# Kernel optimization log

Measured on AMD Instinct MI355X. Metric: run time of the kernel, lower is better.

The kernel has to match this reference:

```python
import jax, jax.numpy as jnp
import numpy as np

NUM_Q_HEADS = 32
NUM_KV_HEADS = 8
HEAD_DIM = 128
HIDDEN = 4096
EPS = 1e-6
ROPE_THETA = 1e6


def _rmsnorm(t, w):
    # per-head RMSNorm over last dim (head_dim), as in skip_rmsnorm with residual=None
    var = jnp.mean(t * t, axis=-1, keepdims=True)
    return t * jax.lax.rsqrt(var + EPS) * w


def _rotate_half(t):
    h = t.shape[-1] // 2
    return jnp.concatenate([-t[..., h:], t[..., :h]], axis=-1)


def setup_inputs() -> dict:
    key = jax.random.key(0)
    ks = jax.random.split(key, 4)
    B, S = 2, 1024
    x = jax.random.normal(ks[0], (B, S, HIDDEN), jnp.float32)
    q_proj_w = jax.random.normal(ks[1], (HIDDEN, NUM_Q_HEADS * HEAD_DIM), jnp.float32) * 0.02
    kv_proj_w = jax.random.normal(ks[2], (HIDDEN, 2 * NUM_KV_HEADS * HEAD_DIM), jnp.float32) * 0.02
    o_proj_w = jax.random.normal(ks[3], (NUM_Q_HEADS * HEAD_DIM, HIDDEN), jnp.float32) * 0.02
    q_norm_w = jnp.ones((HEAD_DIM,), jnp.float32)
    k_norm_w = jnp.ones((HEAD_DIM,), jnp.float32)
    # real rotate-half RoPE tables, shape [S, head_dim]
    inv_freq = 1.0 / (ROPE_THETA ** (jnp.arange(0, HEAD_DIM, 2, dtype=jnp.float32) / HEAD_DIM))
    freqs = jnp.arange(S, dtype=jnp.float32)[:, None] * inv_freq[None, :]  # [S, hd/2]
    emb = jnp.concatenate([freqs, freqs], axis=-1)  # [S, hd]
    cos, sin = jnp.cos(emb), jnp.sin(emb)
    kv_buffer = jnp.zeros((16384, 2 * NUM_KV_HEADS, HEAD_DIM), jnp.float32)
    cur_select_index = jnp.arange(B * S, dtype=jnp.int32)
    return {"x": x, "q_proj_w": q_proj_w, "kv_proj_w": kv_proj_w, "o_proj_w": o_proj_w,
            "q_norm_w": q_norm_w, "k_norm_w": k_norm_w, "cos": cos, "sin": sin,
            "kv_buffer": kv_buffer, "cur_select_index": cur_select_index}


def reference(x, q_proj_w, kv_proj_w, o_proj_w, q_norm_w, k_norm_w, cos, sin, kv_buffer, cur_select_index):
    B, S, _ = x.shape
    T = B * S
    xf = x.reshape(T, HIDDEN)
    # projections (weights stored as [in, out])
    xq = (xf @ q_proj_w).reshape(T, NUM_Q_HEADS, HEAD_DIM)
    xkv = xf @ kv_proj_w
    xk = xkv[:, : NUM_KV_HEADS * HEAD_DIM].reshape(T, NUM_KV_HEADS, HEAD_DIM)
    xv = xkv[:, NUM_KV_HEADS * HEAD_DIM:].reshape(T, NUM_KV_HEADS, HEAD_DIM)
    # per-head RMSNorm (Qwen3 q/k norm)
    xq = _rmsnorm(xq, q_norm_w)
    xk = _rmsnorm(xk, k_norm_w)
    # RoPE (cos/sin are [S, hd], tiled over batch, broadcast over heads)
    cos_t = jnp.tile(cos, (B, 1))[:, None, :]  # [T,1,hd]
    sin_t = jnp.tile(sin, (B, 1))[:, None, :]
    xq = xq * cos_t + _rotate_half(xq) * sin_t
    xk = xk * cos_t + _rotate_half(xk) * sin_t
    # paged KV-cache scatter update (update_kv_buffer)
    combined_kv = jnp.concatenate([xk, xv], axis=1)  # [T, 2*Hk, hd]
    buf = kv_buffer.at[cur_select_index].set(combined_kv)
    # ragged causal flash attention (equal per-request lengths here), GQA expand
    rep = NUM_Q_HEADS // NUM_KV_HEADS
    q = xq.reshape(B, S, NUM_Q_HEADS, HEAD_DIM)
    k = jnp.repeat(xk.reshape(B, S, NUM_KV_HEADS, HEAD_DIM), rep, axis=2)
    v = jnp.repeat(xv.reshape(B, S, NUM_KV_HEADS, HEAD_DIM), rep, axis=2)
    scale = HEAD_DIM ** -0.5
    scores = jnp.einsum('bqhd,bkhd->bhqk', q, k) * scale  # [B,H,S,S]
    causal = jnp.tril(jnp.ones((S, S), bool))
    scores = jnp.where(causal[None, None], scores, jnp.float32(-1e30))
    p = jax.nn.softmax(scores, axis=-1)
    attn = jnp.einsum('bhqk,bkhd->bqhd', p, v).reshape(B, S, NUM_Q_HEADS * HEAD_DIM)
    out = attn @ o_proj_w  # [B,S,hidden]
    return out, buf
```

## Files before the change

kernel.cpp:

```cpp
#include <hip/hip_runtime.h>

typedef float fx4 __attribute__((ext_vector_type(4)));
typedef short s16x4 __attribute__((ext_vector_type(4)));
typedef short s16x8 __attribute__((ext_vector_type(8)));
typedef __bf16 bf16x8 __attribute__((ext_vector_type(8)));

__device__ __forceinline__ short f2bf(float f) {
  unsigned u = __builtin_bit_cast(unsigned, f);
  u += 0x7fffu + ((u >> 16) & 1u);
  return (short)(u >> 16);
}

__device__ __forceinline__ bf16x8 ld8(const short* p) {
  s16x8 v = *(const s16x8*)p;
  return __builtin_bit_cast(bf16x8, v);
}

__device__ __forceinline__ void gld16(const void* g, void* l) {
  __builtin_amdgcn_global_load_lds(
      (const __attribute__((address_space(1))) unsigned*)g,
      (__attribute__((address_space(3))) unsigned*)l, 16, 0, 0);
}

template<int N> __device__ __forceinline__ void wait_vmcnt() {
  if constexpr (N == 0)      asm volatile("s_waitcnt vmcnt(0)" ::: "memory");
  else if constexpr (N == 4) asm volatile("s_waitcnt vmcnt(4)" ::: "memory");
  __builtin_amdgcn_sched_barrier(0);
}

__device__ __forceinline__ void barrier_pin() {
  __builtin_amdgcn_s_barrier();
  __builtin_amdgcn_sched_barrier(0);
}

__global__ __launch_bounds__(256) void cvt_k(const float* __restrict__ in,
                                             short* __restrict__ out) {
  int i = (blockIdx.x * 256 + threadIdx.x) * 8;
  fx4 a = *(const fx4*)(in + i);
  fx4 b = *(const fx4*)(in + i + 4);
  s16x8 w;
  w[0] = f2bf(a[0]); w[1] = f2bf(a[1]); w[2] = f2bf(a[2]); w[3] = f2bf(a[3]);
  w[4] = f2bf(b[0]); w[5] = f2bf(b[1]); w[6] = f2bf(b[2]); w[7] = f2bf(b[3]);
  *(s16x8*)(out + i) = w;
}

__global__ __launch_bounds__(256) void tr_k(const float* __restrict__ in,
    short* __restrict__ out, int K, int N) {
  __shared__ short T[64][72];
  const int ktiles = K >> 6;
  const int tk0 = (blockIdx.x % ktiles) << 6;
  const int tn0 = (blockIdx.x / ktiles) << 6;
  const int tid = threadIdx.x;
  #pragma unroll
  for (int i = 0; i < 4; ++i) {
    int idx = i * 256 + tid;
    int k = idx >> 4, n4 = (idx & 15) << 2;
    fx4 v = *(const fx4*)(in + (size_t)(tk0 + k) * N + tn0 + n4);
    #pragma unroll
    for (int j = 0; j < 4; ++j) T[n4 + j][k] = f2bf(v[j]);
  }
  __syncthreads();
  #pragma unroll
  for (int i = 0; i < 2; ++i) {
    int idx = i * 256 + tid;
    int n = idx >> 3, k8 = (idx & 7) << 3;
    *(s16x8*)(out + (size_t)(tn0 + n) * K + tk0 + k8) = *(const s16x8*)&T[n][k8];
  }
}

__global__ __launch_bounds__(256) void vtr_k(const short* __restrict__ vbp,
                                             short* __restrict__ vbt) {
  __shared__ short T[64][72];
  const int tile = blockIdx.x & 31;
  const int tt = tile & 15, dt = tile >> 4;
  const int bk = blockIdx.x >> 5;
  const int b = bk >> 3, kvh = bk & 7;
  const int t0 = tt << 6, d0 = dt << 6;
  const int tid = threadIdx.x;
  #pragma unroll
  for (int i = 0; i < 2; ++i) {
    int idx = i * 256 + tid;
    int r = idx >> 3, c8 = (idx & 7) << 3;
    s16x8 v = *(const s16x8*)(vbp + (size_t)(b * 1024 + t0 + r) * 1024 + kvh * 128 + d0 + c8);
    #pragma unroll
    for (int j = 0; j < 8; ++j) T[c8 + j][r] = v[j];
  }
  __syncthreads();
  #pragma unroll
  for (int i = 0; i < 2; ++i) {
    int idx = i * 256 + tid;
    int r = idx >> 3, c8 = (idx & 7) << 3;
    *(s16x8*)(vbt + ((size_t)(b * 8 + kvh) * 128 + d0 + r) * 1024 + t0 + c8) =
        *(const s16x8*)&T[r][c8];
  }
}

__global__ __launch_bounds__(512) void gemm8(const short* __restrict__ A,
    const short* __restrict__ Bt, float* __restrict__ Cp, int N, int K) {
  __shared__ short As[2][2][128 * 64];
  __shared__ short Bs[2][2][128 * 64];
  const int tiles_n = N >> 8;
  const int tm = blockIdx.x / tiles_n, tn = blockIdx.x % tiles_n;
  const int tid = threadIdx.x;
  const int lane = tid & 63, wv = tid >> 6;
  const int wm = (wv >> 2) << 6;
  const int wn = (wv & 3) << 5;
  const int r0 = tm << 8, c0 = tn << 8;
  const int lrow = lane & 15, lg = lane >> 4;

  auto stageA = [&](int t, int hh) {
    int k0 = t << 6, s = t & 1;
    #pragma unroll
    for (int i = 0; i < 2; ++i) {
      int c = i * 512 + tid;
      int row = c >> 3, ch = c & 7;
      gld16(A + (size_t)(r0 + hh * 128 + row) * K + k0 + ((ch ^ (row & 7)) << 3),
            &As[s][hh][(i * 512 + wv * 64) * 8]);
    }
  };
  auto stageB = [&](int t, int hh) {
    int k0 = t << 6, s = t & 1;
    #pragma unroll
    for (int i = 0; i < 2; ++i) {
      int c = i * 512 + tid;
      int row = c >> 3, ch = c & 7;
      gld16(Bt + (size_t)(c0 + hh * 128 + row) * K + k0 + ((ch ^ (row & 7)) << 3),
            &Bs[s][hh][(i * 512 + wv * 64) * 8]);
    }
  };

  fx4 acc[2][2][4][2] = {};
  bf16x8 a[4][2], b[2][2];

  auto ldA = [&](int s, int hh) {
    #pragma unroll
    for (int mf = 0; mf < 4; ++mf) {
      int lr = wm + mf * 16 + lrow;
      #pragma unroll
      for (int ks = 0; ks < 2; ++ks)
        a[mf][ks] = ld8(&As[s][hh][lr * 64 + ((((ks << 2) + lg) ^ (lr & 7)) << 3)]);
    }
  };
  auto ldB = [&](int s, int hh) {
    #pragma unroll
    for (int nf = 0; nf < 2; ++nf) {
      int lr = wn + nf * 16 + lrow;
      #pragma unroll
      for (int ks = 0; ks < 2; ++ks)
        b[nf][ks] = ld8(&Bs[s][hh][lr * 64 + ((((ks << 2) + lg) ^ (lr & 7)) << 3)]);
    }
  };

  const int nt = K >> 6;
  stageA(0, 0); stageA(0, 1); stageB(0, 0); stageB(0, 1);
  stageA(1, 0); stageB(1, 1);

  for (int t = 0; t < nt; ++t) {
    const int s = t & 1;
    if (t + 1 < nt) wait_vmcnt<4>(); else wait_vmcnt<0>();
    barrier_pin();
    ldA(s, 0); ldB(s, 0);
    if (t + 1 < nt) stageA(t + 1, 1);
    __builtin_amdgcn_s_setprio(1);
    #pragma unroll
    for (int ks = 0; ks < 2; ++ks)
      #pragma unroll
      for (int mf = 0; mf < 4; ++mf)
        #pragma unroll
        for (int nf = 0; nf < 2; ++nf)
          acc[0][0][mf][nf] = __builtin_amdgcn_mfma_f32_16x16x32_bf16(
              a[mf][ks], b[nf][ks], acc[0][0][mf][nf], 0, 0, 0);
    __builtin_amdgcn_s_setprio(0);
    barrier_pin();
    ldB(s, 1);
    if (t + 1 < nt) stageB(t + 1, 0);
    __builtin_amdgcn_s_setprio(1);
    #pragma unroll
    for (int ks = 0; ks < 2; ++ks)
      #pragma unroll
      for (int mf = 0; mf < 4; ++mf)
        #pragma unroll
        for (int nf = 0; nf < 2; ++nf)
          acc[0][1][mf][nf] = __builtin_amdgcn_mfma_f32_16x16x32_bf16(
              a[mf][ks], b[nf][ks], acc[0][1][mf][nf], 0, 0, 0);
    __builtin_amdgcn_s_setprio(0);
    barrier_pin();
    ldA(s, 1);
    if (t + 2 < nt) stageA(t + 2, 0);
    __builtin_amdgcn_s_setprio(1);
    #pragma unroll
    for (int ks = 0; ks < 2; ++ks)
      #pragma unroll
      for (int mf = 0; mf < 4; ++mf)
        #pragma unroll
        for (int nf = 0; nf < 2; ++nf)
          acc[1][1][mf][nf] = __builtin_amdgcn_mfma_f32_16x16x32_bf16(
              a[mf][ks], b[nf][ks], acc[1][1][mf][nf], 0, 0, 0);
    __builtin_amdgcn_s_setprio(0);
    barrier_pin();
    ldB(s, 0);
    if (t + 2 < nt) stageB(t + 2, 1);
    __builtin_amdgcn_s_setprio(1);
    #pragma unroll
    for (int ks = 0; ks < 2; ++ks)
      #pragma unroll
      for (int mf = 0; mf < 4; ++mf)
        #pragma unroll
        for (int nf = 0; nf < 2; ++nf)
          acc[1][0][mf][nf] = __builtin_amdgcn_mfma_f32_16x16x32_bf16(
              a[mf][ks], b[nf][ks], acc[1][0][mf][nf], 0, 0, 0);
    __builtin_amdgcn_s_setprio(0);
    barrier_pin();
  }
  const int g4 = lg << 2;
  #pragma unroll
  for (int mq = 0; mq < 2; ++mq)
    #pragma unroll
    for (int nq = 0; nq < 2; ++nq)
      #pragma unroll
      for (int mf = 0; mf < 4; ++mf)
        #pragma unroll
        for (int nf = 0; nf < 2; ++nf)
          #pragma unroll
          for (int j = 0; j < 4; ++j) {
            int row = r0 + mq * 128 + wm + mf * 16 + g4 + j;
            int col = c0 + nq * 128 + wn + nf * 16 + lrow;
            Cp[(size_t)row * N + col] = acc[mq][nq][mf][nf][j];
          }
}

__global__ __launch_bounds__(256) void gemm_k(const short* __restrict__ A,
    const short* __restrict__ Bt, float* __restrict__ Cp, int N, int K) {
  __shared__ short As[2][128 * 64];
  __shared__ short Bs[2][128 * 64];
  const int tiles_n = N >> 7;
  const int tm = blockIdx.x / tiles_n, tn = blockIdx.x % tiles_n;
  const int tid = threadIdx.x;
  const int lane = tid & 63, wv = tid >> 6;
  const int wr = (wv >> 1) << 6, wc = (wv & 1) << 6;
  const int r0 = tm << 7, c0 = tn << 7;
  const int lrow = lane & 15, lg = lane >> 4;
  fx4 acc[4][4] = {};

  auto stage = [&](int buf, int k0) {
    #pragma unroll
    for (int i = 0; i < 4; ++i) {
      int c = i * 256 + tid;
      int row = c >> 3, ch = c & 7;
      gld16(A + (size_t)(r0 + row) * K + k0 + ((ch ^ (row & 7)) << 3),
            &As[buf][(i * 256 + wv * 64) * 8]);
    }
    #pragma unroll
    for (int i = 0; i < 4; ++i) {
      int c = i * 256 + tid;
      int row = c >> 3, ch = c & 7;
      gld16(Bt + (size_t)(c0 + row) * K + k0 + ((ch ^ (row & 7)) << 3),
            &Bs[buf][(i * 256 + wv * 64) * 8]);
    }
  };

  const int nt = K >> 6;
  stage(0, 0);
  __syncthreads();
  int cur = 0;
  for (int t = 0; t < nt; ++t) {
    if (t + 1 < nt) stage(cur ^ 1, (t + 1) << 6);
    bf16x8 af[4][2], bfr[4][2];
    #pragma unroll
    for (int m = 0; m < 4; ++m) {
      int row = wr + m * 16 + lrow;
      #pragma unroll
      for (int h = 0; h < 2; ++h)
        af[m][h] = ld8(&As[cur][row * 64 + ((((h << 2) + lg) ^ (row & 7)) << 3)]);
    }
    #pragma unroll
    for (int n = 0; n < 4; ++n) {
      int row = wc + n * 16 + lrow;
      #pragma unroll
      for (int h = 0; h < 2; ++h)
        bfr[n][h] = ld8(&Bs[cur][row * 64 + ((((h << 2) + lg) ^ (row & 7)) << 3)]);
    }
    __builtin_amdgcn_s_setprio(1);
    #pragma unroll
    for (int m = 0; m < 4; ++m)
      #pragma unroll
      for (int n = 0; n < 4; ++n) {
        acc[m][n] = __builtin_amdgcn_mfma_f32_16x16x32_bf16(af[m][0], bfr[n][0], acc[m][n], 0, 0, 0);
        acc[m][n] = __builtin_amdgcn_mfma_f32_16x16x32_bf16(af[m][1], bfr[n][1], acc[m][n], 0, 0, 0);
      }
    __builtin_amdgcn_s_setprio(0);
    __syncthreads();
    cur ^= 1;
  }
  const int g4 = lg << 2;
  #pragma unroll
  for (int m = 0; m < 4; ++m)
    #pragma unroll
    for (int n = 0; n < 4; ++n)
      #pragma unroll
      for (int j = 0; j < 4; ++j) {
        int row = r0 + wr + m * 16 + g4 + j;
        int col = c0 + wc + n * 16 + lrow;
        Cp[(size_t)row * N + col] = acc[m][n][j];
      }
}

__global__ __launch_bounds__(256) void nr_k(const float* __restrict__ xqkv,
    const float* __restrict__ qnw, const float* __restrict__ knw,
    const float* __restrict__ cosb, const float* __restrict__ sinb,
    const int* __restrict__ idx,
    short* __restrict__ qb, short* __restrict__ kbp, short* __restrict__ vbp,
    float* __restrict__ bufo) {
  int rid = blockIdx.x * 4 + (threadIdx.x >> 6);
  int l = threadIdx.x & 63;
  int type, t, h;
  if (rid < 65536)      { type = 0; t = rid >> 5; h = rid & 31; }
  else if (rid < 81920) { type = 1; int r = rid - 65536; t = r >> 3; h = r & 7; }
  else                  { type = 2; int r = rid - 81920; t = r >> 3; h = r & 7; }
  int s = t & 1023;
  const float* src = xqkv + (size_t)t * 6144 +
                     ((type == 0) ? h * 128 : (type == 1) ? 4096 + h * 128
                                                          : 5120 + h * 128);
  float e0 = src[l], e1 = src[l + 64];
  float out0, out1;
  if (type < 2) {
    float ss = e0 * e0 + e1 * e1;
    #pragma unroll
    for (int off = 1; off < 64; off <<= 1) ss += __shfl_xor(ss, off);
    float r = rsqrtf(ss * (1.0f / 128.0f) + 1e-6f);
    const float* nw = (type == 0) ? qnw : knw;
    float n0 = e0 * r * nw[l], n1 = e1 * r * nw[l + 64];
    float c0 = cosb[s * 128 + l], c1 = cosb[s * 128 + 64 + l];
    float s0 = sinb[s * 128 + l], s1 = sinb[s * 128 + 64 + l];
    out0 = n0 * c0 - n1 * s0;
    out1 = n1 * c1 + n0 * s1;
  } else { out0 = e0; out1 = e1; }
  if (type == 0) {
    short* d = qb + (size_t)t * 4096 + h * 128;
    d[l] = f2bf(out0); d[l + 64] = f2bf(out1);
  } else {
    int br = idx[t];
    float* bd = bufo + (size_t)br * 2048 + (type == 1 ? 0 : 1024) + h * 128;
    bd[l] = out0; bd[l + 64] = out1;
    short* d = (type == 1) ? kbp + (size_t)t * 1024 + h * 128
                           : vbp + (size_t)t * 1024 + h * 128;
    d[l] = f2bf(out0); d[l + 64] = f2bf(out1);
  }
}

#define KLD 136
#define PLD 72

__global__ __launch_bounds__(256) void attn_k(const short* __restrict__ qb,
    const short* __restrict__ kbp, const short* __restrict__ vbt,
    short* __restrict__ ob) {
  __shared__ short Ks[64 * KLD];
  __shared__ short Vs[128 * 64];
  __shared__ short Ps[4][16 * PLD];
  const int bid = blockIdx.x;
  const int qt = 15 - (bid & 15), h = (bid >> 4) & 31, b = bid >> 9;
  const int kvh = h >> 2;
  const int tid = threadIdx.x, lane = tid & 63, w = tid >> 6;
  const int lrow = lane & 15, lg = lane >> 4, lk = lg << 3;
  const int q0 = qt << 6;
  const float SC2 = 0.088388347648318447f * 1.4426950408889634f;

  bf16x8 qf[4];
  {
    const short* qp = qb + ((size_t)(b * 1024 + q0 + w * 16 + lrow) * 32 + h) * 128 + lk;
    #pragma unroll
    for (int kb4 = 0; kb4 < 4; ++kb4) qf[kb4] = ld8(qp + kb4 * 32);
  }

  const short* vt_base = vbt + (size_t)(b * 8 + kvh) * 128 * 1024;

  const int sr = tid >> 4, sd8 = (tid & 15) << 3;
  const int vdr = tid >> 3, vch = tid & 7;
  s16x8 kreg[4], vreg[4];
  auto ldkv = [&](int kv0) {
    #pragma unroll
    for (int it = 0; it < 4; ++it) {
      int r = (it << 4) + sr;
      kreg[it] = *(const s16x8*)(kbp + ((size_t)(b * 1024 + kv0 + r) * 8 + kvh) * 128 + sd8);
      int d = (it << 5) + vdr;
      vreg[it] = *(const s16x8*)(vt_base + (size_t)d * 1024 + kv0 + (vch << 3));
    }
  };
  auto wrkv = [&]() {
    #pragma unroll
    for (int it = 0; it < 4; ++it) {
      int r = (it << 4) + sr;
      *(s16x8*)&Ks[r * KLD + sd8] = kreg[it];
      int d = (it << 5) + vdr;
      *(s16x8*)&Vs[d * 64 + ((vch ^ (d & 7)) << 3)] = vreg[it];
    }
  };

  float m[4], lsum[4];
  fx4 acc[8] = {};
  #pragma unroll
  for (int j = 0; j < 4; ++j) { m[j] = -3.0e38f; lsum[j] = 0.f; }

  ldkv(0);
  wrkv();
  __syncthreads();

  for (int kt = 0; kt <= qt; ++kt) {
    const int kv0 = kt << 6;
    if (kt < qt) ldkv((kt + 1) << 6);
    fx4 sf[4];
    #pragma unroll
    for (int nc = 0; nc < 4; ++nc) {
      fx4 z = {0.f, 0.f, 0.f, 0.f};
      sf[nc] = z;
      #pragma unroll
      for (int kb4 = 0; kb4 < 4; ++kb4) {
        bf16x8 kf = ld8(&Ks[(nc * 16 + lrow) * KLD + kb4 * 32 + lk]);
        sf[nc] = __builtin_amdgcn_mfma_f32_16x16x32_bf16(qf[kb4], kf, sf[nc], 0, 0, 0);
      }
    }
    if (kt == qt) {
      #pragma unroll
      for (int nc = 0; nc < 4; ++nc)
        #pragma unroll
        for (int j = 0; j < 4; ++j) {
          int qr = q0 + w * 16 + (lg << 2) + j;
          int kc = kv0 + nc * 16 + lrow;
          if (kc > qr) sf[nc][j] = -3.0e38f;
        }
    }
    float pm[4];
    #pragma unroll
    for (int j = 0; j < 4; ++j) pm[j] = -3.0e38f;
    #pragma unroll
    for (int nc = 0; nc < 4; ++nc)
      #pragma unroll
      for (int j = 0; j < 4; ++j) pm[j] = fmaxf(pm[j], sf[nc][j]);
    #pragma unroll
    for (int j = 0; j < 4; ++j) {
      pm[j] = fmaxf(pm[j], __shfl_xor(pm[j], 1));
      pm[j] = fmaxf(pm[j], __shfl_xor(pm[j], 2));
      pm[j] = fmaxf(pm[j], __shfl_xor(pm[j], 4));
      pm[j] = fmaxf(pm[j], __shfl_xor(pm[j], 8));
    }
    float alpha[4], rs[4];
    #pragma unroll
    for (int j = 0; j < 4; ++j) {
      float mn = fmaxf(m[j], pm[j]);
      alpha[j] = exp2f((m[j] - mn) * SC2);
      m[j] = mn;
      rs[j] = 0.f;
    }
    #pragma unroll
    for (int nc = 0; nc < 4; ++nc)
      #pragma unroll
      for (int j = 0; j < 4; ++j) {
        float p = exp2f((sf[nc][j] - m[j]) * SC2);
        rs[j] += p;
        Ps[w][((lg << 2) + j) * PLD + nc * 16 + lrow] = f2bf(p);
      }
    #pragma unroll
    for (int j = 0; j < 4; ++j) {
      rs[j] += __shfl_xor(rs[j], 1);
      rs[j] += __shfl_xor(rs[j], 2);
      rs[j] += __shfl_xor(rs[j], 4);
      rs[j] += __shfl_xor(rs[j], 8);
      lsum[j] = lsum[j] * alpha[j] + rs[j];
    }
    #pragma unroll
    for (int dg = 0; dg < 8; ++dg)
      #pragma unroll
      for (int j = 0; j < 4; ++j) acc[dg][j] *= alpha[j];
    #pragma unroll
    for (int kb2 = 0; kb2 < 2; ++kb2) {
      bf16x8 pf = ld8(&Ps[w][lrow * PLD + kb2 * 32 + lk]);
      #pragma unroll
      for (int dg = 0; dg < 8; ++dg) {
        int d = dg * 16 + lrow;
        int tch = (kb2 << 2) + lg;
        bf16x8 vf = ld8(&Vs[d * 64 + ((tch ^ (d & 7)) << 3)]);
        acc[dg] = __builtin_amdgcn_mfma_f32_16x16x32_bf16(pf, vf, acc[dg], 0, 0, 0);
      }
    }
    __syncthreads();
    if (kt < qt) {
      wrkv();
      __syncthreads();
    }
  }
  #pragma unroll
  for (int j = 0; j < 4; ++j) {
    float rl = 1.0f / lsum[j];
    int t = b * 1024 + q0 + w * 16 + (lg << 2) + j;
    short* op = ob + ((size_t)t * 32 + h) * 128;
    #pragma unroll
    for (int dg = 0; dg < 8; ++dg)
      op[dg * 16 + lrow] = f2bf(acc[dg][j] * rl);
  }
}

extern "C" void kernel_launch(void* const* d_in, const int* in_sizes, int n_in,
                              void* d_out, int out_size, void* d_ws, size_t ws_size,
                              hipStream_t stream) {
  (void)in_sizes; (void)n_in; (void)out_size; (void)ws_size;
  const float* x    = (const float*)d_in[0];
  const float* qw   = (const float*)d_in[1];
  const float* kvw  = (const float*)d_in[2];
  const float* ow   = (const float*)d_in[3];
  const float* qnw  = (const float*)d_in[4];
  const float* knw  = (const float*)d_in[5];
  const float* cosb = (const float*)d_in[6];
  const float* sinb = (const float*)d_in[7];
  const float* kvbf = (const float*)d_in[8];
  const int*   idx  = (const int*)d_in[9];

  float* outp = (float*)d_out;
  float* bufp = outp + (size_t)2048 * 4096;

  char* ws = (char*)d_ws;
  float* xqkv = (float*)ws;
  short* qb   = (short*)(ws + (size_t)2048 * 6144 * 4);
  short* kbp  = (short*)((char*)qb + (size_t)2048 * 4096 * 2);
  short* vbp  = (short*)((char*)kbp + (size_t)2048 * 1024 * 2);
  short* attnb = (short*)xqkv;
  short* owt   = (short*)((char*)xqkv + (size_t)2048 * 4096 * 2);
  short* vbt   = owt;

  short* wqkvt = (short*)bufp;
  short* xb    = (short*)((char*)bufp + (size_t)6144 * 4096 * 2);

  cvt_k<<<dim3(4096), dim3(256), 0, stream>>>(x, xb);
  tr_k<<<dim3(64 * 64), dim3(256), 0, stream>>>(qw, wqkvt, 4096, 4096);
  tr_k<<<dim3(64 * 32), dim3(256), 0, stream>>>(kvw, wqkvt + (size_t)4096 * 4096, 4096, 2048);
  gemm8<<<dim3(8 * 24), dim3(512), 0, stream>>>(xb, wqkvt, xqkv, 6144, 4096);
  hipMemcpyAsync(bufp + (size_t)2048 * 2048, kvbf + (size_t)2048 * 2048,
                 (size_t)(16384 - 2048) * 2048 * 4, hipMemcpyDeviceToDevice, stream);
  nr_k<<<dim3(98304 / 4), dim3(256), 0, stream>>>(xqkv, qnw, knw, cosb, sinb, idx,
                                                  qb, kbp, vbp, bufp);
  vtr_k<<<dim3(512), dim3(256), 0, stream>>>(vbp, vbt);
  attn_k<<<dim3(2 * 32 * 16), dim3(256), 0, stream>>>(qb, kbp, vbt, attnb);
  tr_k<<<dim3(64 * 64), dim3(256), 0, stream>>>(ow, owt, 4096, 4096);
  gemm_k<<<dim3(16 * 32), dim3(256), 0, stream>>>(attnb, owt, outp, 4096, 4096);
}
```

Baseline: 401.4 us.

## Replace output-projection GEMM with 256x128-tile, 512-thread, triple-buffered pipelined kernel

Replaces the 128x128 double-buffered o_proj GEMM with a 256x128 tile kernel using 8 waves and a three-stage LDS ring. Loads are issued two K-tiles ahead and tracked with explicit vmcnt waits, and each half of the A tile is consumed in its own phase between barriers. The aim is to hide global-load latency behind MFMA work and to reuse each B tile across more rows. In exchange it launches 256 blocks instead of 512, which may under-fill the 256 CUs, and it uses more LDS per block.

```diff
diff --git a/kernel.cpp b/kernel.cpp
--- a/kernel.cpp
+++ b/kernel.cpp
@@ -25,6 +25,7 @@
 template<int N> __device__ __forceinline__ void wait_vmcnt() {
   if constexpr (N == 0)      asm volatile("s_waitcnt vmcnt(0)" ::: "memory");
   else if constexpr (N == 4) asm volatile("s_waitcnt vmcnt(4)" ::: "memory");
+  else if constexpr (N == 6) asm volatile("s_waitcnt vmcnt(6)" ::: "memory");
   __builtin_amdgcn_sched_barrier(0);
 }
 
@@ -229,80 +230,110 @@
           }
 }
 
-__global__ __launch_bounds__(256) void gemm_k(const short* __restrict__ A,
+__global__ __launch_bounds__(512) void gemm4(const short* __restrict__ A,
     const short* __restrict__ Bt, float* __restrict__ Cp, int N, int K) {
-  __shared__ short As[2][128 * 64];
-  __shared__ short Bs[2][128 * 64];
+  __shared__ short As[3][2][128 * 64];
+  __shared__ short Bs[3][128 * 64];
   const int tiles_n = N >> 7;
   const int tm = blockIdx.x / tiles_n, tn = blockIdx.x % tiles_n;
   const int tid = threadIdx.x;
   const int lane = tid & 63, wv = tid >> 6;
-  const int wr = (wv >> 1) << 6, wc = (wv & 1) << 6;
-  const int r0 = tm << 7, c0 = tn << 7;
+  const int wm = (wv >> 2) << 6;
+  const int wn = (wv & 3) << 5;
+  const int r0 = tm << 8, c0 = tn << 7;
   const int lrow = lane & 15, lg = lane >> 4;
-  fx4 acc[4][4] = {};
-
-  auto stage = [&](int buf, int k0) {
-    #pragma unroll
-    for (int i = 0; i < 4; ++i) {
-      int c = i * 256 + tid;
+
+  auto stageA = [&](int t, int hh) {
+    int k0 = t << 6, s = t % 3;
+    #pragma unroll
+    for (int i = 0; i < 2; ++i) {
+      int c = i * 512 + tid;
       int row = c >> 3, ch = c & 7;
-      gld16(A + (size_t)(r0 + row) * K + k0 + ((ch ^ (row & 7)) << 3),
-            &As[buf][(i * 256 + wv * 64) * 8]);
-    }
-    #pragma unroll
-    for (int i = 0; i < 4; ++i) {
-      int c = i * 256 + tid;
+      gld16(A + (size_t)(r0 + hh * 128 + row) * K + k0 + ((ch ^ (row & 7)) << 3),
+            &As[s][hh][(i * 512 + wv * 64) * 8]);
+    }
+  };
+  auto stageB = [&](int t) {
+    int k0 = t << 6, s = t % 3;
+    #pragma unroll
+    for (int i = 0; i < 2; ++i) {
+      int c = i * 512 + tid;
       int row = c >> 3, ch = c & 7;
       gld16(Bt + (size_t)(c0 + row) * K + k0 + ((ch ^ (row & 7)) << 3),
-            &Bs[buf][(i * 256 + wv * 64) * 8]);
+            &Bs[s][(i * 512 + wv * 64) * 8]);
+    }
+  };
+
+  fx4 acc[2][4][2] = {};
+  bf16x8 a[4][2], b[2][2];
+
+  auto ldA = [&](int s, int hh) {
+    #pragma unroll
+    for (int mf = 0; mf < 4; ++mf) {
+      int lr = wm + mf * 16 + lrow;
+      #pragma unroll
+      for (int ks = 0; ks < 2; ++ks)
+        a[mf][ks] = ld8(&As[s][hh][lr * 64 + ((((ks << 2) + lg) ^ (lr & 7)) << 3)]);
+    }
+  };
+  auto ldB = [&](int s) {
+    #pragma unroll
+    for (int nf = 0; nf < 2; ++nf) {
+      int lr = wn + nf * 16 + lrow;
+      #pragma unroll
+      for (int ks = 0; ks < 2; ++ks)
+        b[nf][ks] = ld8(&Bs[s][lr * 64 + ((((ks << 2) + lg) ^ (lr & 7)) << 3)]);
     }
   };
 
   const int nt = K >> 6;
-  stage(0, 0);
-  __syncthreads();
-  int cur = 0;
+  stageA(0, 0); stageA(0, 1); stageB(0);
+  stageA(1, 0); stageA(1, 1); stageB(1);
+
   for (int t = 0; t < nt; ++t) {
-    if (t + 1 < nt) stage(cur ^ 1, (t + 1) << 6);
-    bf16x8 af[4][2], bfr[4][2];
-    #pragma unroll
-    for (int m = 0; m < 4; ++m) {
-      int row = wr + m * 16 + lrow;
-      #pragma unroll
-      for (int h = 0; h < 2; ++h)
-        af[m][h] = ld8(&As[cur][row * 64 + ((((h << 2) + lg) ^ (row & 7)) << 3)]);
-    }
-    #pragma unroll
-    for (int n = 0; n < 4; ++n) {
-      int row = wc + n * 16 + lrow;
-      #pragma unroll
-      for (int h = 0; h < 2; ++h)
-        bfr[n][h] = ld8(&Bs[cur][row * 64 + ((((h << 2) + lg) ^ (row & 7)) << 3)]);
-    }
+    const int s = t % 3;
+    if (t + 1 < nt) wait_vmcnt<6>(); else wait_vmcnt<0>();
+    barrier_pin();
+    ldA(s, 0); ldB(s);
+    if (t + 2 < nt) stageA(t + 2, 0);
     __builtin_amdgcn_s_setprio(1);
     #pragma unroll
-    for (int m = 0; m < 4; ++m)
-      #pragma unroll
-      for (int n = 0; n < 4; ++n) {
-        acc[m][n] = __builtin_amdgcn_mfma_f32_16x16x32_bf16(af[m][0], bfr[n][0], acc[m][n], 0, 0, 0);
-        acc[m][n] = __builtin_amdgcn_mfma_f32_16x16x32_bf16(af[m][1], bfr[n][1], acc[m][n], 0, 0, 0);
-      }
+    for (int ks = 0; ks < 2; ++ks)
+      #pragma unroll
+      for (int mf = 0; mf < 4; ++mf)
+        #pragma unroll
+        for (int nf = 0; nf < 2; ++nf)
+          acc[0][mf][nf] = __builtin_amdgcn_mfma_f32_16x16x32_bf16(
+              a[mf][ks], b[nf][ks], acc[0][mf][nf], 0, 0, 0);
     __builtin_amdgcn_s_setprio(0);
-    __syncthreads();
-    cur ^= 1;
+    barrier_pin();
+    ldA(s, 1);
+    if (t + 2 < nt) { stageA(t + 2, 1); stageB(t + 2); }
+    __builtin_amdgcn_s_setprio(1);
+    #pragma unroll
+    for (int ks = 0; ks < 2; ++ks)
+      #pragma unroll
+      for (int mf = 0; mf < 4; ++mf)
+        #pragma unroll
+        for (int nf = 0; nf < 2; ++nf)
+          acc[1][mf][nf] = __builtin_amdgcn_mfma_f32_16x16x32_bf16(
+              a[mf][ks], b[nf][ks], acc[1][mf][nf], 0, 0, 0);
+    __builtin_amdgcn_s_setprio(0);
+    barrier_pin();
   }
   const int g4 = lg << 2;
   #pragma unroll
-  for (int m = 0; m < 4; ++m)
-    #pragma unroll
-    for (int n = 0; n < 4; ++n)
-      #pragma unroll
-      for (int j = 0; j < 4; ++j) {
-        int row = r0 + wr + m * 16 + g4 + j;
-        int col = c0 + wc + n * 16 + lrow;
-        Cp[(size_t)row * N + col] = acc[m][n][j];
-      }
+  for (int mh = 0; mh < 2; ++mh)
+    #pragma unroll
+    for (int mf = 0; mf < 4; ++mf)
+      #pragma unroll
+      for (int nf = 0; nf < 2; ++nf)
+        #pragma unroll
+        for (int j = 0; j < 4; ++j) {
+          int row = r0 + mh * 128 + wm + mf * 16 + g4 + j;
+          int col = c0 + wn + nf * 16 + lrow;
+          Cp[(size_t)row * N + col] = acc[mh][mf][nf][j];
+        }
 }
 
 __global__ __launch_bounds__(256) void nr_k(const float* __restrict__ xqkv,
@@ -540,5 +571,5 @@
   vtr_k<<<dim3(512), dim3(256), 0, stream>>>(vbp, vbt);
   attn_k<<<dim3(2 * 32 * 16), dim3(256), 0, stream>>>(qb, kbp, vbt, attnb);
   tr_k<<<dim3(64 * 64), dim3(256), 0, stream>>>(ow, owt, 4096, 4096);
-  gemm_k<<<dim3(16 * 32), dim3(256), 0, stream>>>(attnb, owt, outp, 4096, 4096);
-}
+  gemm4<<<dim3(8 * 32), dim3(512), 0, stream>>>(attnb, owt, outp, 4096, 4096);
+}
```

Measured after the change: 398.6 us. Within noise of the previous version (-0.7%).
